# Kernel tuning notes

Hardware: AMD Instinct MI355X
Metric: run time of the kernel (lower is better)

Reference implementation:

```python
import jax, jax.numpy as jnp
import numpy as np


def setup_inputs() -> dict:
    key = jax.random.key(0)
    B, N = 128, 512
    SSMap = jax.random.normal(key, (B, N, N), dtype=jnp.float32)
    return {"SSMap": SSMap}


def reference(SSMap):
    # SSMap: [B, N, N]. For each superdiagonal offset d = 1..N-2 (length L = N-d,
    # the final length-1 diagonal is excluded), compute unbiased std of
    # (diag * L / 5) = std(diag) * L / 5, then mean over diagonals per batch item.
    B, N, _ = SSMap.shape
    K = N - 2  # number of diagonals used (offsets 1..N-2)
    P = N - 1  # max diagonal length
    k = jnp.arange(K)[:, None]            # diagonal index -> offset d = k+1
    p = jnp.arange(P)[None, :]            # position along diagonal
    rows = jnp.broadcast_to(p, (K, P))    # row index i = p
    cols = p + k + 1                      # col index j = p + d
    mask = cols < N                       # valid positions: p < N - d
    cols = jnp.minimum(cols, N - 1)
    diags = SSMap[:, rows, cols]          # [B, K, P] padded diagonals
    maskf = mask.astype(SSMap.dtype)      # [K, P]
    lens = jnp.sum(maskf, axis=1)         # [K], L = N - 1 - k (>= 2)
    mean = jnp.sum(diags * maskf, axis=2) / lens            # [B, K]
    dev = (diags - mean[:, :, None]) * maskf                # masked deviations
    var = jnp.sum(dev * dev, axis=2) / (lens - 1.0)         # unbiased (ddof=1)
    scaled = jnp.sqrt(var) * lens / 5.0                     # std(diag * L / 5)
    loss = jnp.mean(scaled, axis=1)                         # [B]
    return (loss, jax.lax.stop_gradient(loss))
```

## Files before the change

### kernel.cpp

```cpp
#include <hip/hip_runtime.h>
#include <math.h>

constexpr int B_ = 128;
constexpr int N_ = 512;
constexpr int K_ = 510;
constexpr int SPLIT = 16;

__global__ __launch_bounds__(256) void diag_partial_kernel(
    const float* __restrict__ in, float* __restrict__ ws) {
  const int b = blockIdx.x / SPLIT;
  const int s = blockIdx.x % SPLIT;
  const int t = threadIdx.x;
  const float* base = in + (size_t)b * N_ * N_;
  const int la = (N_ - 1) - t;
  const int lb = t;
  float Sa0 = 0.f, Qa0 = 0.f, Sa1 = 0.f, Qa1 = 0.f;
  float Sb0 = 0.f, Qb0 = 0.f, Sb1 = 0.f, Qb1 = 0.f;

  {
    const int r0 = 16 * s;
    const float* pa = base + (size_t)r0 * (N_ + 1) + 1 + t;
    const float* pb = base + (size_t)r0 * (N_ + 1) + (N_ - t);
#pragma unroll
    for (int i = 0; i < 16; i += 2) {
      const int p0 = r0 + i;
      const int p1 = r0 + i + 1;
      float a0 = pa[0];
      float a1 = pa[N_ + 1];
      float b0 = (p0 < lb) ? pb[0] : 0.f;
      float b1 = (p1 < lb) ? pb[N_ + 1] : 0.f;
      Sa0 += a0; Qa0 = fmaf(a0, a0, Qa0);
      Sa1 += a1; Qa1 = fmaf(a1, a1, Qa1);
      Sb0 += b0; Qb0 = fmaf(b0, b0, Qb0);
      Sb1 += b1; Qb1 = fmaf(b1, b1, Qb1);
      pa += 2 * (N_ + 1);
      pb += 2 * (N_ + 1);
    }
  }
  {
    const int r0 = (N_ - 16) - 16 * s;
    const float* pa = base + (size_t)r0 * (N_ + 1) + 1 + t;
#pragma unroll
    for (int i = 0; i < 16; i += 2) {
      const int p0 = r0 + i;
      const int p1 = r0 + i + 1;
      float a0 = (p0 < la) ? pa[0] : 0.f;
      float a1 = (p1 < la) ? pa[N_ + 1] : 0.f;
      Sa0 += a0; Qa0 = fmaf(a0, a0, Qa0);
      Sa1 += a1; Qa1 = fmaf(a1, a1, Qa1);
      pa += 2 * (N_ + 1);
    }
  }

  float* w = ws + (size_t)blockIdx.x * (2 * N_);
  w[t] = Sa0 + Sa1;
  w[t + N_] = Qa0 + Qa1;
  w[(N_ - 1) - t] = Sb0 + Sb1;
  w[(N_ - 1) - t + N_] = Qb0 + Qb1;
}

__global__ __launch_bounds__(512) void finalize_kernel(
    const float* __restrict__ ws, float* __restrict__ out) {
  __shared__ float red[8];
  const int b = blockIdx.x;
  const int t = threadIdx.x;
  float Ssum = 0.0f, Qsum = 0.0f;
#pragma unroll
  for (int s = 0; s < SPLIT; ++s) {
    const float* w = ws + (size_t)(b * SPLIT + s) * (2 * N_);
    Ssum += w[t];
    Qsum += w[t + N_];
  }
  float scaled = 0.0f;
  if (t < K_) {
    float len = (float)(N_ - 1 - t);
    float mean = Ssum / len;
    float var = (Qsum - Ssum * mean) / (len - 1.0f);
    var = fmaxf(var, 0.0f);
    scaled = sqrtf(var) * len * 0.2f;
  }
  for (int off = 32; off > 0; off >>= 1)
    scaled += __shfl_down(scaled, off, 64);
  const int wid = t >> 6;
  if ((t & 63) == 0) red[wid] = scaled;
  __syncthreads();
  if (t == 0) {
    float tot = 0.0f;
    for (int i = 0; i < 8; ++i) tot += red[i];
    float loss = tot / (float)K_;
    out[b] = loss;
    out[B_ + b] = loss;
  }
}

extern "C" void kernel_launch(void* const* d_in, const int* in_sizes, int n_in,
                              void* d_out, int out_size, void* d_ws, size_t ws_size,
                              hipStream_t stream) {
  const float* in = (const float*)d_in[0];
  float* out = (float*)d_out;
  float* ws = (float*)d_ws;
  diag_partial_kernel<<<B_ * SPLIT, 256, 0, stream>>>(in, ws);
  finalize_kernel<<<B_, 512, 0, stream>>>(ws, out);
}
```

Before: 184.6 us.

## Stage row tiles in LDS with float4 coalesced loads before diagonal accumulation

Instead of each thread reading strided diagonal elements directly from global memory, each block now loads its 16-row upper-triangle slabs into shared memory with vectorized float4 row-major loads. It skips 64-column chunks that lie below the diagonal, then reads the diagonals from LDS. This targets the poorly coalesced diagonal-stride global accesses. In exchange it adds LDS traffic, barriers and about 33KB of shared memory per block, which may reduce occupancy.

```diff
diff --git a/kernel.cpp b/kernel.cpp
--- a/kernel.cpp
+++ b/kernel.cpp
@@ -5,58 +5,80 @@
 constexpr int N_ = 512;
 constexpr int K_ = 510;
 constexpr int SPLIT = 16;
+constexpr int PAD = 520;
+
+typedef float float4v __attribute__((ext_vector_type(4)));
 
 __global__ __launch_bounds__(256) void diag_partial_kernel(
     const float* __restrict__ in, float* __restrict__ ws) {
-  const int b = blockIdx.x / SPLIT;
-  const int s = blockIdx.x % SPLIT;
+  __shared__ float L[16 * PAD];
+  const int b = blockIdx.x >> 4;
+  const int s = blockIdx.x & 15;
   const int t = threadIdx.x;
   const float* base = in + (size_t)b * N_ * N_;
-  const int la = (N_ - 1) - t;
-  const int lb = t;
-  float Sa0 = 0.f, Qa0 = 0.f, Sa1 = 0.f, Qa1 = 0.f;
-  float Sb0 = 0.f, Qb0 = 0.f, Sb1 = 0.f, Qb1 = 0.f;
+
+  float Sa = 0.f, Qa = 0.f, Sb = 0.f, Qb = 0.f;
 
   {
-    const int r0 = 16 * s;
-    const float* pa = base + (size_t)r0 * (N_ + 1) + 1 + t;
-    const float* pb = base + (size_t)r0 * (N_ + 1) + (N_ - t);
+    const int rA = 16 * s;
+    const int q = t & 127;
+    const int half = t >> 7;
 #pragma unroll
-    for (int i = 0; i < 16; i += 2) {
-      const int p0 = r0 + i;
-      const int p1 = r0 + i + 1;
-      float a0 = pa[0];
-      float a1 = pa[N_ + 1];
-      float b0 = (p0 < lb) ? pb[0] : 0.f;
-      float b1 = (p1 < lb) ? pb[N_ + 1] : 0.f;
-      Sa0 += a0; Qa0 = fmaf(a0, a0, Qa0);
-      Sa1 += a1; Qa1 = fmaf(a1, a1, Qa1);
-      Sb0 += b0; Qb0 = fmaf(b0, b0, Qb0);
-      Sb1 += b1; Qb1 = fmaf(b1, b1, Qb1);
-      pa += 2 * (N_ + 1);
-      pb += 2 * (N_ + 1);
+    for (int j = 0; j < 8; ++j) {
+      const int i = 2 * j + half;
+      const int p = rA + i;
+      const int c0 = (p + 1) & ~63;
+      const int col = 4 * q;
+      if (col >= c0) {
+        const float4v v = *(const float4v*)(base + (size_t)p * N_ + col);
+        *(float4v*)&L[i * PAD + col] = v;
+      }
     }
+    __syncthreads();
+#pragma unroll
+    for (int i = 0; i < 16; ++i) {
+      const int p = rA + i;
+      const float xa = L[i * PAD + (p + 1 + t)];
+      Sa += xa; Qa = fmaf(xa, xa, Qa);
+      const int cb = p + 512 - t;
+      float xb = L[i * PAD + (cb < PAD ? cb : PAD - 1)];
+      xb = (t > p) ? xb : 0.f;
+      Sb += xb; Qb = fmaf(xb, xb, Qb);
+    }
+    __syncthreads();
   }
+
   {
-    const int r0 = (N_ - 16) - 16 * s;
-    const float* pa = base + (size_t)r0 * (N_ + 1) + 1 + t;
+    const int rB = (N_ - 16) - 16 * s;
+    const int q = t & 63;
+    const int quarter = t >> 6;
 #pragma unroll
-    for (int i = 0; i < 16; i += 2) {
-      const int p0 = r0 + i;
-      const int p1 = r0 + i + 1;
-      float a0 = (p0 < la) ? pa[0] : 0.f;
-      float a1 = (p1 < la) ? pa[N_ + 1] : 0.f;
-      Sa0 += a0; Qa0 = fmaf(a0, a0, Qa0);
-      Sa1 += a1; Qa1 = fmaf(a1, a1, Qa1);
-      pa += 2 * (N_ + 1);
+    for (int j = 0; j < 4; ++j) {
+      const int i = 4 * j + quarter;
+      const int p = rB + i;
+      const int c0 = (p + 1) & ~63;
+      const int col = 256 + 4 * q;
+      if (col >= c0) {
+        const float4v v = *(const float4v*)(base + (size_t)p * N_ + col);
+        *(float4v*)&L[i * PAD + col] = v;
+      }
+    }
+    __syncthreads();
+#pragma unroll
+    for (int i = 0; i < 16; ++i) {
+      const int p = rB + i;
+      const int ca = p + 1 + t;
+      float xa = L[i * PAD + (ca < PAD ? ca : PAD - 1)];
+      xa = (t < N_ - 1 - p) ? xa : 0.f;
+      Sa += xa; Qa = fmaf(xa, xa, Qa);
     }
   }
 
   float* w = ws + (size_t)blockIdx.x * (2 * N_);
-  w[t] = Sa0 + Sa1;
-  w[t + N_] = Qa0 + Qa1;
-  w[(N_ - 1) - t] = Sb0 + Sb1;
-  w[(N_ - 1) - t + N_] = Qb0 + Qb1;
+  w[t] = Sa;
+  w[t + N_] = Qa;
+  w[(N_ - 1) - t] = Sb;
+  w[(N_ - 1) - t + N_] = Qb;
 }
 
 __global__ __launch_bounds__(512) void finalize_kernel(
```

Measured after the change: 195.6 us. 1.06x slower.
